# Optimization experiments

Hardware: AMD Instinct MI355X
Metric: run time of the kernel (lower is better)

Reference implementation:

```python
import jax, jax.numpy as jnp
import numpy as np

B, N, D, H = 4, 2048, 512, 8
DH = D // H
EPS = 1e-6


def setup_inputs() -> dict:
    key = jax.random.key(0)
    ks = jax.random.split(key, 12)
    s = 1.0 / np.sqrt(D)
    return {
        "x": jax.random.normal(ks[0], (B, N, D), jnp.float32),
        "attn_bias": jax.random.normal(ks[1], (B, 1, N, N), jnp.float32),
        "Wq": jax.random.normal(ks[2], (D, D), jnp.float32) * s,
        "bq": jnp.zeros((D,), jnp.float32),
        "Wk": jax.random.normal(ks[3], (D, D), jnp.float32) * s,
        "bk": jnp.zeros((D,), jnp.float32),
        "Wv": jax.random.normal(ks[4], (D, D), jnp.float32) * s,
        "bv": jnp.zeros((D,), jnp.float32),
        "Wo": jax.random.normal(ks[5], (D, D), jnp.float32) * s,
        "bo": jnp.zeros((D,), jnp.float32),
        "q_gamma": jnp.ones((DH,), jnp.float32),
        "q_beta": jnp.zeros((DH,), jnp.float32),
        "k_gamma": jnp.ones((DH,), jnp.float32),
        "k_beta": jnp.zeros((DH,), jnp.float32),
    }


def _layernorm(x, gamma, beta):
    mu = jnp.mean(x, axis=-1, keepdims=True)
    var = jnp.var(x, axis=-1, keepdims=True)
    return (x - mu) * jax.lax.rsqrt(var + EPS) * gamma + beta


def reference(x, attn_bias, Wq, bq, Wk, bk, Wv, bv, Wo, bo,
              q_gamma, q_beta, k_gamma, k_beta):
    b, n, d = x.shape
    # project and split heads: (B, H, N, DH)
    def heads(W, bias):
        return (x @ W.T + bias).reshape(b, n, H, DH).transpose(0, 2, 1, 3)
    q = heads(Wq, bq)
    k = heads(Wk, bk)
    v = heads(Wv, bv)
    q = _layernorm(q, q_gamma, q_beta)
    k = _layernorm(k, k_gamma, k_beta)
    scores = jnp.einsum('bhqd,bhkd->bhqk', q, k) / np.sqrt(DH)
    scores = scores + attn_bias  # (B,1,N,N) broadcasts over heads
    attn = jax.nn.softmax(scores, axis=-1)
    out = jnp.einsum('bhqk,bhkd->bhqd', attn, v)
    out = out.transpose(0, 2, 1, 3).reshape(b, n, d)
    return out @ Wo.T + bo
```

## Files before the change

### kernel.cpp

```cpp
#include <hip/hip_runtime.h>

typedef __attribute__((ext_vector_type(8))) short short8;
typedef __attribute__((ext_vector_type(4))) float f32x4;
typedef __attribute__((ext_vector_type(4))) int i32x4;
typedef __attribute__((ext_vector_type(4))) unsigned short u16x4;
typedef __attribute__((ext_vector_type(8))) unsigned short u16x8;
typedef __attribute__((ext_vector_type(2))) unsigned int u32x2;

#define B_  4
#define N_  2048
#define D_  512
#define H_  8
#define DH_ 64
#define M_  (B_ * N_)

__device__ __forceinline__ float bf2f(unsigned short s) {
    union { unsigned u; float f; } un; un.u = ((unsigned)s) << 16; return un.f;
}
__device__ __forceinline__ unsigned short f2bf(float f) {
    union { float f; unsigned u; } un; un.f = f;
    unsigned r = un.u + 0x7FFFu + ((un.u >> 16) & 1u);
    return (unsigned short)(r >> 16);
}
__device__ __forceinline__ unsigned packbf(float lo, float hi) {
    union { float f; unsigned u; } a, b;
    a.f = lo; b.f = hi;
    return __builtin_amdgcn_perm(b.u + 0x8000u, a.u + 0x8000u, 0x07060302u);
}
__device__ __forceinline__ float lo16f(unsigned u) {
    union { unsigned u; float f; } un; un.u = u << 16; return un.f;
}
__device__ __forceinline__ float hi16f(unsigned u) {
    union { unsigned u; float f; } un; un.u = u & 0xFFFF0000u; return un.f;
}

typedef __attribute__((address_space(1))) const void gvoid;
typedef __attribute__((address_space(3))) void svoid;
__device__ __forceinline__ void load16_lds(const void* g, void* s) {
    __builtin_amdgcn_global_load_lds((gvoid*)g, (svoid*)s, 16, 0, 0);
}

__global__ __launch_bounds__(256) void cvt_x(const float* __restrict__ src,
                                             unsigned short* __restrict__ dst) {
    const int i = (blockIdx.x * 256 + threadIdx.x) * 4;
    f32x4 v = *(const f32x4*)(src + i);
    u16x4 o;
    o[0] = f2bf(v[0]); o[1] = f2bf(v[1]); o[2] = f2bf(v[2]); o[3] = f2bf(v[3]);
    *(u16x4*)(dst + i) = o;
}

__global__ __launch_bounds__(256) void cvt_bias(const float* __restrict__ src,
                                                unsigned short* __restrict__ dst) {
    const size_t i = ((size_t)blockIdx.x * 256 + threadIdx.x) * 8;
    const int kv = (int)(i & 2047);
    const int q  = (int)((i >> 11) & 2047);
    const int b  = (int)(i >> 22);
    f32x4 v0 = *(const f32x4*)(src + i);
    f32x4 v1 = *(const f32x4*)(src + i + 4);
    u16x8 o;
    o[0] = f2bf(v0[0]); o[1] = f2bf(v0[1]); o[2] = f2bf(v0[2]); o[3] = f2bf(v0[3]);
    o[4] = f2bf(v1[0]); o[5] = f2bf(v1[1]); o[6] = f2bf(v1[2]); o[7] = f2bf(v1[3]);
    const size_t oi = ((((size_t)b * 64 + (q >> 5)) * 32 + (kv >> 6)) * 32 + (q & 31)) * 64 + (kv & 63);
    *(u16x8*)(dst + oi) = o;
}

__global__ __launch_bounds__(256) void cvt_w(const float* __restrict__ W0,
                                             const float* __restrict__ W1,
                                             const float* __restrict__ W2,
                                             const float* __restrict__ W3,
                                             unsigned short* __restrict__ dst) {
    const int sel = blockIdx.y;
    const float* src = (sel == 0) ? W0 : (sel == 1) ? W1 : (sel == 2) ? W2 : W3;
    unsigned short* d = dst + (size_t)sel * D_ * D_;
    const int i = (blockIdx.x * 256 + threadIdx.x) * 4;
    f32x4 v = *(const f32x4*)(src + i);
    u16x4 o;
    o[0] = f2bf(v[0]); o[1] = f2bf(v[1]); o[2] = f2bf(v[2]); o[3] = f2bf(v[3]);
    *(u16x4*)(d + i) = o;
}

template <bool F32OUT, bool LNF>
__global__ __launch_bounds__(256, 2) void gemm_nt(
    const unsigned short* __restrict__ A,
    const unsigned short* __restrict__ W,
    const float* __restrict__ Bv0,
    const float* __restrict__ Bv1,
    const float* __restrict__ Bv2,
    const float* __restrict__ g0, const float* __restrict__ be0,
    const float* __restrict__ g1, const float* __restrict__ be1,
    unsigned short* __restrict__ outb,
    float* __restrict__ outf)
{
    const int mt = blockIdx.x;
    const int nt = blockIdx.y;
    const int sel = nt >> 2;
    const unsigned short* Wp = W + (size_t)sel * D_ * D_;
    const float* Bv = (sel == 0) ? Bv0 : (sel == 1) ? Bv1 : Bv2;
    const int n0 = (nt & 3) * 128;

    __shared__ __align__(16) unsigned short As[128 * 32];
    __shared__ __align__(16) unsigned short Bs[128 * 32];

    const int tid = threadIdx.x;
    const int w   = tid >> 6;
    const int l   = tid & 63;
    const int l15 = l & 15;
    const int qd  = l >> 4;
    const int wr  = w >> 1;
    const int wc  = w & 1;

    int srow[2], scol[2];
#pragma unroll
    for (int c = 0; c < 2; ++c) {
        const int g   = (w * 2 + c) * 64 + l;
        const int row = g >> 2;
        srow[c] = row;
        scol[c] = ((g & 3) ^ (row & 3)) * 8;
    }

    f32x4 acc[4][4];
#pragma unroll
    for (int i = 0; i < 4; ++i)
#pragma unroll
        for (int j = 0; j < 4; ++j)
            acc[i][j] = (f32x4){0.f, 0.f, 0.f, 0.f};

    const int swz = qd ^ (l15 & 3);

    for (int k0 = 0; k0 < D_; k0 += 32) {
        __syncthreads();
#pragma unroll
        for (int c = 0; c < 2; ++c) {
            load16_lds(A  + (size_t)(mt * 128 + srow[c]) * D_ + k0 + scol[c],
                       As + (w * 2 + c) * 512);
            load16_lds(Wp + (size_t)(n0 + srow[c]) * D_ + k0 + scol[c],
                       Bs + (w * 2 + c) * 512);
        }
        __syncthreads();

        short8 af[4], bfr[4];
#pragma unroll
        for (int rt = 0; rt < 4; ++rt)
            af[rt] = *(const short8*)&As[(wr * 64 + rt * 16 + l15) * 32 + swz * 8];
#pragma unroll
        for (int ct = 0; ct < 4; ++ct)
            bfr[ct] = *(const short8*)&Bs[(wc * 64 + ct * 16 + l15) * 32 + swz * 8];
#pragma unroll
        for (int rt = 0; rt < 4; ++rt)
#pragma unroll
            for (int ct = 0; ct < 4; ++ct)
                acc[rt][ct] = __builtin_amdgcn_mfma_f32_16x16x32_bf16(
                    af[rt], bfr[ct], acc[rt][ct], 0, 0, 0);
    }

    const float* gam = (sel == 0) ? g0 : g1;
    const float* bet = (sel == 0) ? be0 : be1;
    float gv[4], bv2[4];
    if (LNF) {
#pragma unroll
        for (int ct = 0; ct < 4; ++ct) { gv[ct] = gam[ct * 16 + l15]; bv2[ct] = bet[ct * 16 + l15]; }
    }

#pragma unroll
    for (int rt = 0; rt < 4; ++rt) {
        float v[4][4];
#pragma unroll
        for (int ct = 0; ct < 4; ++ct) {
            const float bias = Bv[n0 + wc * 64 + ct * 16 + l15];
#pragma unroll
            for (int r = 0; r < 4; ++r) v[ct][r] = acc[rt][ct][r] + bias;
        }
        if (LNF && sel < 2) {
#pragma unroll
            for (int r = 0; r < 4; ++r) {
                float s  = v[0][r] + v[1][r] + v[2][r] + v[3][r];
                float s2 = v[0][r]*v[0][r] + v[1][r]*v[1][r] + v[2][r]*v[2][r] + v[3][r]*v[3][r];
#pragma unroll
                for (int o = 1; o <= 8; o <<= 1) {
                    s  += __shfl_xor(s, o);
                    s2 += __shfl_xor(s2, o);
                }
                const float mu  = s * 0.015625f;
                const float var = s2 * 0.015625f - mu * mu;
                const float rs  = rsqrtf(var + 1e-6f);
#pragma unroll
                for (int ct = 0; ct < 4; ++ct)
                    v[ct][r] = (v[ct][r] - mu) * rs * gv[ct] + bv2[ct];
            }
        }
#pragma unroll
        for (int ct = 0; ct < 4; ++ct) {
            const int col  = n0 + wc * 64 + ct * 16 + l15;
            const int row0 = mt * 128 + wr * 64 + rt * 16 + qd * 4;
#pragma unroll
            for (int r = 0; r < 4; ++r) {
                const size_t oidx = (size_t)(row0 + r) * D_ + col;
                if (F32OUT) outf[oidx] = v[ct][r];
                else        outb[(size_t)sel * M_ * D_ + oidx] = f2bf(v[ct][r]);
            }
        }
    }
}

__global__ __launch_bounds__(256) void pack_kv(
    const unsigned short* __restrict__ K, const unsigned short* __restrict__ V,
    unsigned short* __restrict__ Kt, unsigned short* __restrict__ Vt2)
{
    const int nt = blockIdx.x, b = blockIdx.y;
    const int tid = threadIdx.x;
    __shared__ __align__(16) unsigned short Vl[64][520];

#pragma unroll
    for (int i = 0; i < 16; ++i) {
        const int c = i * 256 + tid;
        const int row = c >> 6, ch = c & 63;
        const size_t srow = ((size_t)(b * N_ + nt * 64 + row)) * D_ + ch * 8;
        i32x4 kd = *(const i32x4*)(K + srow);
        const int h = ch >> 3, dc = ch & 7;
        *(i32x4*)(Kt + ((((size_t)(b * 8 + h) * 32 + nt) * 64 + row) * 64) + dc * 8) = kd;
        i32x4 vd = *(const i32x4*)(V + srow);
        *(i32x4*)&Vl[row][ch * 8] = vd;
    }
    __syncthreads();
#pragma unroll
    for (int i = 0; i < 16; ++i) {
        const int c = i * 256 + tid;
        const int h = c >> 9, r = c & 511;
        const int dh = r >> 3, kc = r & 7;
        u16x8 o;
#pragma unroll
        for (int j = 0; j < 8; ++j) o[j] = Vl[kc * 8 + j][h * 64 + dh];
        *(u16x8*)(Vt2 + ((((size_t)(b * 8 + h) * 32 + nt) * 64 + dh) * 64) + kc * 8) = o;
    }
}

__global__ __launch_bounds__(256, 3) void attn7(
    const unsigned short* __restrict__ Qm,
    const unsigned short* __restrict__ Kt,
    const unsigned short* __restrict__ Vt2,
    const unsigned short* __restrict__ Bt,
    unsigned short* __restrict__ AO)
{
    const int qt = blockIdx.x;
    const int h  = blockIdx.y;
    const int b  = blockIdx.z;
    const int w  = threadIdx.x >> 6;
    const int l  = threadIdx.x & 63;
    const int l15 = l & 15;
    const int qd  = l >> 4;
    const int q0 = qt * 128 + w * 32;

    __shared__ __align__(16) unsigned char smem[51200];
    unsigned char* Kb = smem;
    unsigned char* Vb = smem + 8192;
    unsigned char* Bb = smem + 16384 + w * 4096;
    unsigned short* PwB = (unsigned short*)(smem + 32768) + w * 32 * 72;

    short8 qf[2][2];
#pragma unroll
    for (int ct = 0; ct < 2; ++ct)
#pragma unroll
        for (int hf = 0; hf < 2; ++hf)
            qf[ct][hf] = *(const short8*)(Qm +
                (size_t)(b * N_ + q0 + ct * 16 + l15) * D_ + h * DH_ + hf * 32 + qd * 8);

    f32x4 Ot[4][2];
#pragma unroll
    for (int rt = 0; rt < 4; ++rt)
#pragma unroll
        for (int ct = 0; ct < 2; ++ct) Ot[rt][ct] = (f32x4){0.f, 0.f, 0.f, 0.f};
    float m_i[2] = {-3.0e38f, -3.0e38f};
    float l_i[2] = {0.f, 0.f};

    const unsigned short* Ktile0 = Kt  + (((size_t)(b * 8 + h) * 32) * 64) * 64;
    const unsigned short* Vtile0 = Vt2 + (((size_t)(b * 8 + h) * 32) * 64) * 64;
    const unsigned short* Btile0 = Bt  + (((size_t)b * 64 + qt * 4 + w) * 32) * 2048;

    for (int kt = 0; kt < 32; ++kt) {
        const unsigned short* Ktile = Ktile0 + (size_t)kt * 4096;
        const unsigned short* Vtile = Vtile0 + (size_t)kt * 4096;
        const unsigned short* Btile = Btile0 + (size_t)kt * 2048;

        __syncthreads();
#pragma unroll
        for (int i = 0; i < 2; ++i) {
            const int c = (w * 2 + i) * 64 + l;
            const int row = c >> 3, g = c & 7;
            const int sg = g ^ (row & 7);
            load16_lds(Ktile + row * 64 + sg * 8, Kb + c * 16);
            load16_lds(Vtile + row * 64 + sg * 8, Vb + c * 16);
        }
#pragma unroll
        for (int i = 0; i < 4; ++i) {
            const int c = i * 64 + l;
            const int q = c >> 3, g = c & 7;
            const int sg = g ^ (q & 7);
            load16_lds(Btile + q * 64 + sg * 8, Bb + c * 16);
        }
        __syncthreads();

        short8 kf[4][2];
#pragma unroll
        for (int rt = 0; rt < 4; ++rt) {
            const int kv = rt * 16 + l15;
#pragma unroll
            for (int hf = 0; hf < 2; ++hf) {
                const int cidx = (hf * 4 + qd) ^ (kv & 7);
                kf[rt][hf] = *(const short8*)(Kb + kv * 128 + cidx * 16);
            }
        }

        f32x4 St[4][2];
#pragma unroll
        for (int rt = 0; rt < 4; ++rt)
#pragma unroll
            for (int ct = 0; ct < 2; ++ct) {
                f32x4 v = (f32x4){0.f, 0.f, 0.f, 0.f};
                v = __builtin_amdgcn_mfma_f32_16x16x32_bf16(kf[rt][0], qf[ct][0], v, 0, 0, 0);
                v = __builtin_amdgcn_mfma_f32_16x16x32_bf16(kf[rt][1], qf[ct][1], v, 0, 0, 0);
                St[rt][ct] = v;
            }

        u32x2 braw[4][2];
#pragma unroll
        for (int rt = 0; rt < 4; ++rt)
#pragma unroll
            for (int ct = 0; ct < 2; ++ct) {
                const int q = ct * 16 + l15;
                const int cidx = (rt * 2 + (qd >> 1)) ^ (q & 7);
                braw[rt][ct] = *(const u32x2*)(Bb + q * 128 + cidx * 16 + (qd & 1) * 8);
            }

        short8 vf[4][2];
#pragma unroll
        for (int rt = 0; rt < 4; ++rt) {
            const int dh = rt * 16 + l15;
#pragma unroll
            for (int hf = 0; hf < 2; ++hf) {
                const int cidx = (hf * 4 + qd) ^ (dh & 7);
                vf[rt][hf] = *(const short8*)(Vb + dh * 128 + cidx * 16);
            }
        }

#pragma unroll
        for (int ct = 0; ct < 2; ++ct) {
            float sv[4][4];
            float mx = -3.0e38f;
#pragma unroll
            for (int rt = 0; rt < 4; ++rt) {
                sv[rt][0] = St[rt][ct][0] * 0.125f + lo16f(braw[rt][ct][0]);
                sv[rt][1] = St[rt][ct][1] * 0.125f + hi16f(braw[rt][ct][0]);
                sv[rt][2] = St[rt][ct][2] * 0.125f + lo16f(braw[rt][ct][1]);
                sv[rt][3] = St[rt][ct][3] * 0.125f + hi16f(braw[rt][ct][1]);
#pragma unroll
                for (int r = 0; r < 4; ++r) mx = fmaxf(mx, sv[rt][r]);
            }
            mx = fmaxf(mx, __shfl_xor(mx, 16));
            mx = fmaxf(mx, __shfl_xor(mx, 32));
            const float mnew  = fmaxf(m_i[ct], mx);
            const float alpha = __expf(m_i[ct] - mnew);
            float rsum = 0.f;
#pragma unroll
            for (int rt = 0; rt < 4; ++rt) {
                const float p0 = __expf(sv[rt][0] - mnew), p1 = __expf(sv[rt][1] - mnew);
                const float p2 = __expf(sv[rt][2] - mnew), p3 = __expf(sv[rt][3] - mnew);
                rsum += (p0 + p1) + (p2 + p3);
                u32x2 pw; pw[0] = packbf(p0, p1); pw[1] = packbf(p2, p3);
                *(u32x2*)&PwB[(ct * 16 + l15) * 72 + rt * 16 + qd * 4] = pw;
            }
            l_i[ct] = l_i[ct] * alpha + rsum;
            m_i[ct] = mnew;
#pragma unroll
            for (int rt = 0; rt < 4; ++rt)
#pragma unroll
                for (int r = 0; r < 4; ++r) Ot[rt][ct][r] *= alpha;
        }

        short8 pf[2][2];
#pragma unroll
        for (int ct = 0; ct < 2; ++ct)
#pragma unroll
            for (int hf = 0; hf < 2; ++hf)
                pf[ct][hf] = *(const short8*)&PwB[(ct * 16 + l15) * 72 + hf * 32 + qd * 8];

#pragma unroll
        for (int rt = 0; rt < 4; ++rt)
#pragma unroll
            for (int ct = 0; ct < 2; ++ct) {
                Ot[rt][ct] = __builtin_amdgcn_mfma_f32_16x16x32_bf16(vf[rt][0], pf[ct][0], Ot[rt][ct], 0, 0, 0);
                Ot[rt][ct] = __builtin_amdgcn_mfma_f32_16x16x32_bf16(vf[rt][1], pf[ct][1], Ot[rt][ct], 0, 0, 0);
            }
    }

#pragma unroll
    for (int ct = 0; ct < 2; ++ct) {
        l_i[ct] += __shfl_xor(l_i[ct], 16);
        l_i[ct] += __shfl_xor(l_i[ct], 32);
        const float inv = 1.f / l_i[ct];
        const int q = q0 + ct * 16 + l15;
#pragma unroll
        for (int rt = 0; rt < 4; ++rt) {
            u16x4 ob;
#pragma unroll
            for (int r = 0; r < 4; ++r) ob[r] = f2bf(Ot[rt][ct][r] * inv);
            *(u16x4*)(AO + (size_t)(b * N_ + q) * D_ + h * DH_ + rt * 16 + qd * 4) = ob;
        }
    }
}

extern "C" void kernel_launch(void* const* d_in, const int* in_sizes, int n_in,
                              void* d_out, int out_size, void* d_ws, size_t ws_size,
                              hipStream_t stream) {
    const float* x  = (const float*)d_in[0];
    const float* ab = (const float*)d_in[1];
    const float* Wq = (const float*)d_in[2];
    const float* bq = (const float*)d_in[3];
    const float* Wk = (const float*)d_in[4];
    const float* bk = (const float*)d_in[5];
    const float* Wv = (const float*)d_in[6];
    const float* bv = (const float*)d_in[7];
    const float* Wo = (const float*)d_in[8];
    const float* bo = (const float*)d_in[9];
    const float* qg = (const float*)d_in[10];
    const float* qb = (const float*)d_in[11];
    const float* kg = (const float*)d_in[12];
    const float* kb = (const float*)d_in[13];

    unsigned short* xb  = (unsigned short*)d_ws;
    unsigned short* Wb  = xb  + (size_t)M_ * D_;
    unsigned short* Y   = Wb  + (size_t)4 * D_ * D_;
    unsigned short* Kt  = Y   + (size_t)3 * M_ * D_;
    unsigned short* Vt2 = Kt  + (size_t)M_ * D_;
    unsigned short* AO  = Vt2 + (size_t)M_ * D_;
    unsigned short* Bt  = AO  + (size_t)M_ * D_;
    float* out = (float*)d_out;

    cvt_x<<<dim3(M_ * D_ / 1024), dim3(256), 0, stream>>>(x, xb);
    cvt_w<<<dim3(D_ * D_ / 1024, 4), dim3(256), 0, stream>>>(Wq, Wk, Wv, Wo, Wb);
    cvt_bias<<<dim3((int)((size_t)B_ * N_ * N_ / 2048)), dim3(256), 0, stream>>>(ab, Bt);

    gemm_nt<false, true><<<dim3(64, 12), dim3(256), 0, stream>>>(
        xb, Wb, bq, bk, bv, qg, qb, kg, kb, Y, nullptr);

    pack_kv<<<dim3(32, 4), dim3(256), 0, stream>>>(
        Y + (size_t)M_ * D_, Y + (size_t)2 * M_ * D_, Kt, Vt2);

    attn7<<<dim3(16, 8, 4), dim3(256), 0, stream>>>(
        Y, Kt, Vt2, Bt, AO);

    gemm_nt<true, false><<<dim3(64, 4), dim3(256), 0, stream>>>(
        AO, Wb + (size_t)3 * D_ * D_, bo, bo, bo,
        nullptr, nullptr, nullptr, nullptr, nullptr, out);
}
```

Baseline: 273.7 us.

## Double-buffer K/V tiles and register-prefetch bias in attention, use exp2

Restructures the attention loop into a two-stage software pipeline: K/V tiles for the next step are loaded into an alternate LDS buffer while the current one is consumed, and the bias tile is prefetched straight into registers instead of going through LDS. The bias is pre-scaled by log2(e) during conversion and the QK scale folded so softmax can use the native exp2 instruction. MFMA sections get raised wave priority and the launch bound drops to 2 waves-per-SIMD occupancy. This trades a single barrier pair per tile for more registers and lower occupancy.

```diff
diff --git a/kernel.cpp b/kernel.cpp
--- a/kernel.cpp
+++ b/kernel.cpp
@@ -14,9 +14,6 @@
 #define DH_ 64
 #define M_  (B_ * N_)
 
-__device__ __forceinline__ float bf2f(unsigned short s) {
-    union { unsigned u; float f; } un; un.u = ((unsigned)s) << 16; return un.f;
-}
 __device__ __forceinline__ unsigned short f2bf(float f) {
     union { float f; unsigned u; } un; un.f = f;
     unsigned r = un.u + 0x7FFFu + ((un.u >> 16) & 1u);
@@ -32,6 +29,13 @@
 }
 __device__ __forceinline__ float hi16f(unsigned u) {
     union { unsigned u; float f; } un; un.u = u & 0xFFFF0000u; return un.f;
+}
+__device__ __forceinline__ float exp2fast(float x) {
+#if __has_builtin(__builtin_amdgcn_exp2f)
+    return __builtin_amdgcn_exp2f(x);
+#else
+    float r; asm("v_exp_f32 %0, %1" : "=v"(r) : "v"(x)); return r;
+#endif
 }
 
 typedef __attribute__((address_space(1))) const void gvoid;
@@ -55,11 +59,14 @@
     const int kv = (int)(i & 2047);
     const int q  = (int)((i >> 11) & 2047);
     const int b  = (int)(i >> 22);
+    const float L2E = 1.4426950408889634f;
     f32x4 v0 = *(const f32x4*)(src + i);
     f32x4 v1 = *(const f32x4*)(src + i + 4);
     u16x8 o;
-    o[0] = f2bf(v0[0]); o[1] = f2bf(v0[1]); o[2] = f2bf(v0[2]); o[3] = f2bf(v0[3]);
-    o[4] = f2bf(v1[0]); o[5] = f2bf(v1[1]); o[6] = f2bf(v1[2]); o[7] = f2bf(v1[3]);
+    o[0] = f2bf(v0[0] * L2E); o[1] = f2bf(v0[1] * L2E);
+    o[2] = f2bf(v0[2] * L2E); o[3] = f2bf(v0[3] * L2E);
+    o[4] = f2bf(v1[0] * L2E); o[5] = f2bf(v1[1] * L2E);
+    o[6] = f2bf(v1[2] * L2E); o[7] = f2bf(v1[3] * L2E);
     const size_t oi = ((((size_t)b * 64 + (q >> 5)) * 32 + (kv >> 6)) * 32 + (q & 31)) * 64 + (kv & 63);
     *(u16x8*)(dst + oi) = o;
 }
@@ -234,7 +241,7 @@
     }
 }
 
-__global__ __launch_bounds__(256, 3) void attn7(
+__global__ __launch_bounds__(256, 2) void attn8(
     const unsigned short* __restrict__ Qm,
     const unsigned short* __restrict__ Kt,
     const unsigned short* __restrict__ Vt2,
@@ -251,10 +258,16 @@
     const int q0 = qt * 128 + w * 32;
 
     __shared__ __align__(16) unsigned char smem[51200];
-    unsigned char* Kb = smem;
-    unsigned char* Vb = smem + 8192;
-    unsigned char* Bb = smem + 16384 + w * 4096;
     unsigned short* PwB = (unsigned short*)(smem + 32768) + w * 32 * 72;
+
+    int sc[2], soff[2];
+#pragma unroll
+    for (int i = 0; i < 2; ++i) {
+        const int c = (w * 2 + i) * 64 + l;
+        const int row = c >> 3, g = c & 7;
+        sc[i] = c;
+        soff[i] = row * 64 + (g ^ (row & 7)) * 8;
+    }
 
     short8 qf[2][2];
 #pragma unroll
@@ -276,121 +289,135 @@
     const unsigned short* Vtile0 = Vt2 + (((size_t)(b * 8 + h) * 32) * 64) * 64;
     const unsigned short* Btile0 = Bt  + (((size_t)b * 64 + qt * 4 + w) * 32) * 2048;
 
-    for (int kt = 0; kt < 32; ++kt) {
-        const unsigned short* Ktile = Ktile0 + (size_t)kt * 4096;
-        const unsigned short* Vtile = Vtile0 + (size_t)kt * 4096;
-        const unsigned short* Btile = Btile0 + (size_t)kt * 2048;
-
-        __syncthreads();
-#pragma unroll
-        for (int i = 0; i < 2; ++i) {
-            const int c = (w * 2 + i) * 64 + l;
-            const int row = c >> 3, g = c & 7;
-            const int sg = g ^ (row & 7);
-            load16_lds(Ktile + row * 64 + sg * 8, Kb + c * 16);
-            load16_lds(Vtile + row * 64 + sg * 8, Vb + c * 16);
-        }
-#pragma unroll
-        for (int i = 0; i < 4; ++i) {
-            const int c = i * 64 + l;
-            const int q = c >> 3, g = c & 7;
-            const int sg = g ^ (q & 7);
-            load16_lds(Btile + q * 64 + sg * 8, Bb + c * 16);
-        }
-        __syncthreads();
-
-        short8 kf[4][2];
-#pragma unroll
-        for (int rt = 0; rt < 4; ++rt) {
-            const int kv = rt * 16 + l15;
-#pragma unroll
-            for (int hf = 0; hf < 2; ++hf) {
-                const int cidx = (hf * 4 + qd) ^ (kv & 7);
-                kf[rt][hf] = *(const short8*)(Kb + kv * 128 + cidx * 16);
-            }
-        }
-
-        f32x4 St[4][2];
-#pragma unroll
-        for (int rt = 0; rt < 4; ++rt)
-#pragma unroll
-            for (int ct = 0; ct < 2; ++ct) {
-                f32x4 v = (f32x4){0.f, 0.f, 0.f, 0.f};
-                v = __builtin_amdgcn_mfma_f32_16x16x32_bf16(kf[rt][0], qf[ct][0], v, 0, 0, 0);
-                v = __builtin_amdgcn_mfma_f32_16x16x32_bf16(kf[rt][1], qf[ct][1], v, 0, 0, 0);
-                St[rt][ct] = v;
-            }
-
-        u32x2 braw[4][2];
-#pragma unroll
-        for (int rt = 0; rt < 4; ++rt)
-#pragma unroll
-            for (int ct = 0; ct < 2; ++ct) {
-                const int q = ct * 16 + l15;
-                const int cidx = (rt * 2 + (qd >> 1)) ^ (q & 7);
-                braw[rt][ct] = *(const u32x2*)(Bb + q * 128 + cidx * 16 + (qd & 1) * 8);
-            }
-
-        short8 vf[4][2];
-#pragma unroll
-        for (int rt = 0; rt < 4; ++rt) {
-            const int dh = rt * 16 + l15;
-#pragma unroll
-            for (int hf = 0; hf < 2; ++hf) {
-                const int cidx = (hf * 4 + qd) ^ (dh & 7);
-                vf[rt][hf] = *(const short8*)(Vb + dh * 128 + cidx * 16);
-            }
-        }
-
-#pragma unroll
-        for (int ct = 0; ct < 2; ++ct) {
-            float sv[4][4];
-            float mx = -3.0e38f;
-#pragma unroll
-            for (int rt = 0; rt < 4; ++rt) {
-                sv[rt][0] = St[rt][ct][0] * 0.125f + lo16f(braw[rt][ct][0]);
-                sv[rt][1] = St[rt][ct][1] * 0.125f + hi16f(braw[rt][ct][0]);
-                sv[rt][2] = St[rt][ct][2] * 0.125f + lo16f(braw[rt][ct][1]);
-                sv[rt][3] = St[rt][ct][3] * 0.125f + hi16f(braw[rt][ct][1]);
-#pragma unroll
-                for (int r = 0; r < 4; ++r) mx = fmaxf(mx, sv[rt][r]);
-            }
-            mx = fmaxf(mx, __shfl_xor(mx, 16));
-            mx = fmaxf(mx, __shfl_xor(mx, 32));
-            const float mnew  = fmaxf(m_i[ct], mx);
-            const float alpha = __expf(m_i[ct] - mnew);
-            float rsum = 0.f;
-#pragma unroll
-            for (int rt = 0; rt < 4; ++rt) {
-                const float p0 = __expf(sv[rt][0] - mnew), p1 = __expf(sv[rt][1] - mnew);
-                const float p2 = __expf(sv[rt][2] - mnew), p3 = __expf(sv[rt][3] - mnew);
-                rsum += (p0 + p1) + (p2 + p3);
-                u32x2 pw; pw[0] = packbf(p0, p1); pw[1] = packbf(p2, p3);
-                *(u32x2*)&PwB[(ct * 16 + l15) * 72 + rt * 16 + qd * 4] = pw;
-            }
-            l_i[ct] = l_i[ct] * alpha + rsum;
-            m_i[ct] = mnew;
-#pragma unroll
-            for (int rt = 0; rt < 4; ++rt)
-#pragma unroll
-                for (int r = 0; r < 4; ++r) Ot[rt][ct][r] *= alpha;
-        }
-
-        short8 pf[2][2];
+#pragma unroll
+    for (int i = 0; i < 2; ++i) {
+        load16_lds(Ktile0 + soff[i], smem + sc[i] * 16);
+        load16_lds(Vtile0 + soff[i], smem + 8192 + sc[i] * 16);
+    }
+    u32x2 brA[4][2], brB[4][2];
+#pragma unroll
+    for (int rt = 0; rt < 4; ++rt)
 #pragma unroll
         for (int ct = 0; ct < 2; ++ct)
-#pragma unroll
-            for (int hf = 0; hf < 2; ++hf)
-                pf[ct][hf] = *(const short8*)&PwB[(ct * 16 + l15) * 72 + hf * 32 + qd * 8];
-
-#pragma unroll
-        for (int rt = 0; rt < 4; ++rt)
-#pragma unroll
-            for (int ct = 0; ct < 2; ++ct) {
-                Ot[rt][ct] = __builtin_amdgcn_mfma_f32_16x16x32_bf16(vf[rt][0], pf[ct][0], Ot[rt][ct], 0, 0, 0);
-                Ot[rt][ct] = __builtin_amdgcn_mfma_f32_16x16x32_bf16(vf[rt][1], pf[ct][1], Ot[rt][ct], 0, 0, 0);
-            }
-    }
+            brA[rt][ct] = *(const u32x2*)(Btile0 + (ct * 16 + l15) * 64 + rt * 16 + qd * 4);
+    asm volatile("s_waitcnt vmcnt(0)" ::: "memory");
+
+#define ATTN_ITER(KT, CUR, BRC, BRN) do {                                      \
+    unsigned char* Kbc = smem + (CUR) * 16384;                                 \
+    unsigned char* Vbc = Kbc + 8192;                                           \
+    asm volatile("s_waitcnt vmcnt(8)" ::: "memory");                           \
+    __builtin_amdgcn_s_barrier();                                              \
+    __builtin_amdgcn_sched_barrier(0);                                         \
+    if ((KT) < 31) {                                                           \
+        const unsigned short* Kn = Ktile0 + (size_t)((KT) + 1) * 4096;         \
+        const unsigned short* Vn = Vtile0 + (size_t)((KT) + 1) * 4096;         \
+        unsigned char* KbN = smem + (((CUR) ^ 1)) * 16384;                     \
+        _Pragma("unroll")                                                      \
+        for (int i = 0; i < 2; ++i) {                                          \
+            load16_lds(Kn + soff[i], KbN + sc[i] * 16);                        \
+            load16_lds(Vn + soff[i], KbN + 8192 + sc[i] * 16);                 \
+        }                                                                      \
+    }                                                                          \
+    asm volatile("" ::: "memory");       \
+    {                                                                          \
+        const unsigned short* Bn = Btile0 +                                    \
+            (size_t)(((KT) < 31) ? (KT) + 1 : 31) * 2048;                      \
+        _Pragma("unroll")                                                      \
+        for (int rt = 0; rt < 4; ++rt)                                         \
+            _Pragma("unroll")                                                  \
+            for (int ct = 0; ct < 2; ++ct)                                     \
+                BRN[rt][ct] = *(const u32x2*)(Bn + (ct * 16 + l15) * 64 +      \
+                                              rt * 16 + qd * 4);               \
+    }                                                                          \
+    short8 kf[4][2];                                                           \
+    _Pragma("unroll")                                                          \
+    for (int rt = 0; rt < 4; ++rt) {                                           \
+        const int kv = rt * 16 + l15;                                          \
+        _Pragma("unroll")                                                      \
+        for (int hf = 0; hf < 2; ++hf) {                                       \
+            const int cidx = (hf * 4 + qd) ^ (kv & 7);                         \
+            kf[rt][hf] = *(const short8*)(Kbc + kv * 128 + cidx * 16);         \
+        }                                                                      \
+    }                                                                          \
+    f32x4 St[4][2];                                                            \
+    __builtin_amdgcn_s_setprio(1);                                             \
+    _Pragma("unroll")                                                          \
+    for (int rt = 0; rt < 4; ++rt)                                             \
+        _Pragma("unroll")                                                      \
+        for (int ct = 0; ct < 2; ++ct) {                                       \
+            f32x4 v = (f32x4){0.f, 0.f, 0.f, 0.f};                             \
+            v = __builtin_amdgcn_mfma_f32_16x16x32_bf16(kf[rt][0], qf[ct][0], v, 0, 0, 0); \
+            v = __builtin_amdgcn_mfma_f32_16x16x32_bf16(kf[rt][1], qf[ct][1], v, 0, 0, 0); \
+            St[rt][ct] = v;                                                    \
+        }                                                                      \
+    __builtin_amdgcn_s_setprio(0);                                             \
+    short8 vf[4][2];                                                           \
+    _Pragma("unroll")                                                          \
+    for (int rt = 0; rt < 4; ++rt) {                                           \
+        const int dh = rt * 16 + l15;                                          \
+        _Pragma("unroll")                                                      \
+        for (int hf = 0; hf < 2; ++hf) {                                       \
+            const int cidx = (hf * 4 + qd) ^ (dh & 7);                         \
+            vf[rt][hf] = *(const short8*)(Vbc + dh * 128 + cidx * 16);         \
+        }                                                                      \
+    }                                                                          \
+    _Pragma("unroll")                                                          \
+    for (int ct = 0; ct < 2; ++ct) {                                           \
+        float sv[4][4];                                                        \
+        float mx = -3.0e38f;                                                   \
+        _Pragma("unroll")                                                      \
+        for (int rt = 0; rt < 4; ++rt) {                                       \
+            sv[rt][0] = St[rt][ct][0] * 0.1803368801f + lo16f(BRC[rt][ct][0]); \
+            sv[rt][1] = St[rt][ct][1] * 0.1803368801f + hi16f(BRC[rt][ct][0]); \
+            sv[rt][2] = St[rt][ct][2] * 0.1803368801f + lo16f(BRC[rt][ct][1]); \
+            sv[rt][3] = St[rt][ct][3] * 0.1803368801f + hi16f(BRC[rt][ct][1]); \
+            _Pragma("unroll")                                                  \
+            for (int r = 0; r < 4; ++r) mx = fmaxf(mx, sv[rt][r]);             \
+        }                                                                      \
+        mx = fmaxf(mx, __shfl_xor(mx, 16));                                    \
+        mx = fmaxf(mx, __shfl_xor(mx, 32));                                    \
+        const float mnew  = fmaxf(m_i[ct], mx);                                \
+        const float alpha = exp2fast(m_i[ct] - mnew);                          \
+        float rsum = 0.f;                                                      \
+        _Pragma("unroll")                                                      \
+        for (int rt = 0; rt < 4; ++rt) {                                       \
+            const float p0 = exp2fast(sv[rt][0] - mnew);                       \
+            const float p1 = exp2fast(sv[rt][1] - mnew);                       \
+            const float p2 = exp2fast(sv[rt][2] - mnew);                       \
+            const float p3 = exp2fast(sv[rt][3] - mnew);                       \
+            rsum += (p0 + p1) + (p2 + p3);                                     \
+            u32x2 pw; pw[0] = packbf(p0, p1); pw[1] = packbf(p2, p3);          \
+            *(u32x2*)&PwB[(ct * 16 + l15) * 72 + rt * 16 + qd * 4] = pw;       \
+        }                                                                      \
+        l_i[ct] = l_i[ct] * alpha + rsum;                                      \
+        m_i[ct] = mnew;                                                        \
+        _Pragma("unroll")                                                      \
+        for (int rt = 0; rt < 4; ++rt)                                         \
+            _Pragma("unroll")                                                  \
+            for (int r = 0; r < 4; ++r) Ot[rt][ct][r] *= alpha;                \
+    }                                                                          \
+    short8 pf[2][2];                                                           \
+    _Pragma("unroll")                                                          \
+    for (int ct = 0; ct < 2; ++ct)                                             \
+        _Pragma("unroll")                                                      \
+        for (int hf = 0; hf < 2; ++hf)                                         \
+            pf[ct][hf] = *(const short8*)&PwB[(ct * 16 + l15) * 72 + hf * 32 + qd * 8]; \
+    __builtin_amdgcn_s_setprio(1);                                             \
+    _Pragma("unroll")                                                          \
+    for (int rt = 0; rt < 4; ++rt)                                             \
+        _Pragma("unroll")                                                      \
+        for (int ct = 0; ct < 2; ++ct) {                                       \
+            Ot[rt][ct] = __builtin_amdgcn_mfma_f32_16x16x32_bf16(vf[rt][0], pf[ct][0], Ot[rt][ct], 0, 0, 0); \
+            Ot[rt][ct] = __builtin_amdgcn_mfma_f32_16x16x32_bf16(vf[rt][1], pf[ct][1], Ot[rt][ct], 0, 0, 0); \
+        }                                                                      \
+    __builtin_amdgcn_s_setprio(0);                                             \
+} while (0)
+
+    for (int kt2 = 0; kt2 < 16; ++kt2) {
+        ATTN_ITER(kt2 * 2,     0, brA, brB);
+        ATTN_ITER(kt2 * 2 + 1, 1, brB, brA);
+    }
+#undef ATTN_ITER
 
 #pragma unroll
     for (int ct = 0; ct < 2; ++ct) {
@@ -445,7 +472,7 @@
     pack_kv<<<dim3(32, 4), dim3(256), 0, stream>>>(
         Y + (size_t)M_ * D_, Y + (size_t)2 * M_ * D_, Kt, Vt2);
 
-    attn7<<<dim3(16, 8, 4), dim3(256), 0, stream>>>(
+    attn8<<<dim3(16, 8, 4), dim3(256), 0, stream>>>(
         Y, Kt, Vt2, Bt, AO);
 
     gemm_nt<true, false><<<dim3(64, 4), dim3(256), 0, stream>>>(
```

New measurement: 268.9 us. Within noise of the previous version (-1.8%).
